# Kernel tuning notes

Measured on AMD Instinct MI355X. Metric: run time of the kernel, lower is better.

Reference implementation:

```python
import jax, jax.numpy as jnp
import numpy as np

N = 100000   # nodes
E = 1600000  # edges (before self loops)
H = 4        # heads
C = 32       # per-head channels
D = H * C    # hidden_dim = 128
G = 64       # graphs in batch
L = 4        # num_layers
IN_DIM = 7
NEG_SLOPE = 0.2


def setup_inputs() -> dict:
    key = jax.random.key(0)
    ks = jax.random.split(key, 14)
    s = 0.1
    x = jax.random.normal(ks[0], (N, IN_DIM), jnp.float32)
    edge_index = jax.random.randint(ks[1], (2, E), 0, N, dtype=jnp.int32)
    batch = jnp.sort(jax.random.randint(ks[2], (N,), 0, G, dtype=jnp.int32))
    W0 = jax.random.normal(ks[3], (IN_DIM, D), jnp.float32) * s
    a_src0 = jax.random.normal(ks[4], (H, C), jnp.float32) * s
    a_dst0 = jax.random.normal(ks[5], (H, C), jnp.float32) * s
    b0 = jnp.zeros((D,), jnp.float32)
    Ws = jax.random.normal(ks[6], (L - 1, D, D), jnp.float32) * s
    a_srcs = jax.random.normal(ks[7], (L - 1, H, C), jnp.float32) * s
    a_dsts = jax.random.normal(ks[8], (L - 1, H, C), jnp.float32) * s
    bs = jnp.zeros((L - 1, D), jnp.float32)
    ln_g = jnp.ones((L, D), jnp.float32)
    ln_b = jnp.zeros((L, D), jnp.float32)
    return dict(x=x, edge_index=edge_index, batch=batch, W0=W0, a_src0=a_src0,
                a_dst0=a_dst0, b0=b0, Ws=Ws, a_srcs=a_srcs, a_dsts=a_dsts,
                bs=bs, ln_g=ln_g, ln_b=ln_b)


def _gat_layer(x, W, a_src, a_dst, b, src, dst):
    # x: [N, F_in] -> h: [N, H, C] (PyG GATConv: shared lin for src/dst)
    h = (x @ W).reshape(N, H, C)
    alpha_src = jnp.einsum('nhc,hc->nh', h, a_src)  # [N, H]
    alpha_dst = jnp.einsum('nhc,hc->nh', h, a_dst)  # [N, H]
    logits = jax.nn.leaky_relu(alpha_src[src] + alpha_dst[dst], NEG_SLOPE)  # [E', H]
    # segment softmax over edges grouped by destination node
    m = jax.ops.segment_max(logits, dst, num_segments=N)          # [N, H]
    e = jnp.exp(logits - m[dst])
    z = jax.ops.segment_sum(e, dst, num_segments=N)               # [N, H]
    alpha = e / (z[dst] + 1e-16)                                  # [E', H]
    msg = h[src] * alpha[..., None]                               # [E', H, C]
    out = jax.ops.segment_sum(msg, dst, num_segments=N)           # [N, H, C]
    return out.reshape(N, D) + b


def _layernorm(x, g, b):
    mu = jnp.mean(x, axis=-1, keepdims=True)
    var = jnp.var(x, axis=-1, keepdims=True)
    return (x - mu) * jax.lax.rsqrt(var + 1e-5) * g + b


def reference(x, edge_index, batch, W0, a_src0, a_dst0, b0, Ws, a_srcs, a_dsts, bs, ln_g, ln_b):
    # PyG GATConv default: add self loops
    loop = jnp.arange(N, dtype=edge_index.dtype)
    src = jnp.concatenate([edge_index[0], loop])
    dst = jnp.concatenate([edge_index[1], loop])
    h = x
    for i in range(L):
        if i == 0:
            W, asr, ads, b = W0, a_src0, a_dst0, b0
        else:
            W, asr, ads, b = Ws[i - 1], a_srcs[i - 1], a_dsts[i - 1], bs[i - 1]
        h_new = _gat_layer(h, W, asr, ads, b, src, dst)
        h_new = jax.nn.elu(_layernorm(h_new, ln_g[i], ln_b[i]))
        h = h + h_new if i > 0 else h_new  # dropout is identity in eval
    node_embeddings = h  # [N, D]
    sums = jax.ops.segment_sum(node_embeddings, batch, num_segments=G)  # [G, D]
    cnt = jax.ops.segment_sum(jnp.ones((N,), node_embeddings.dtype), batch, num_segments=G)
    graph_embedding = sums / jnp.maximum(cnt, 1.0)[:, None]
    return node_embeddings, graph_embedding
```

## Files before the change

### kernel.cpp

```cpp
#include <hip/hip_runtime.h>
#include <hip/hip_bf16.h>

#define NN 100000
#define NE 1600000
#define NH 4
#define NC 32
#define DD 128
#define NG 64
#define NIN 7

#define BSH 9
#define NBUK ((NN + 511) >> BSH)
#define SEGCAP 9600
#define CAPE (SEGCAP - 512)
#define CSRN (NBUK * SEGCAP)
#define NBBIN ((NE + 4095)/4096)

typedef __hip_bfloat16 bf16;
typedef __attribute__((ext_vector_type(8))) short short8;
typedef __attribute__((ext_vector_type(4))) float f32x4;
typedef __attribute__((ext_vector_type(2))) float f32x2;

__device__ __forceinline__ float b2f(const bf16 v){ return __bfloat162float(v); }

__device__ __forceinline__ float in_ld(const void* p, size_t i, int f32){
  return f32 ? ((const float*)p)[i] : b2f(((const bf16*)p)[i]);
}

__device__ __forceinline__ unsigned int bfbits(float v){
  bf16 b = __float2bfloat16(v);
  return (unsigned int)(*(unsigned short*)&b);
}

__global__ __launch_bounds__(256) void k_init(float* __restrict__ gsum, int* __restrict__ gcnt,
                                              int* __restrict__ bcur,
                                              const unsigned int* __restrict__ xb, int* __restrict__ flag){
  int i = blockIdx.x*256 + threadIdx.x;
  if (i < NG*DD) gsum[i] = 0.f;
  if (i < NG) gcnt[i] = 0;
  if (i < NBUK) bcur[i] = i * CAPE;
  if (blockIdx.x == 0 && threadIdx.x < 64){
    int t = threadIdx.x;
    int pl = 0;
    for (int j = t; j < 512; j += 64){
      float v = __uint_as_float(xb[j]);
      float a = fabsf(v);
      if (v == v && a < 1e6f && a > 1e-10f) pl++;
    }
    #pragma unroll
    for (int off = 32; off > 0; off >>= 1) pl += __shfl_down(pl, off);
    if (t == 0) *flag = (pl >= 384) ? 1 : 0;
  }
}

__global__ __launch_bounds__(256) void k_bin(const int* __restrict__ src, const int* __restrict__ dst,
                                             int* __restrict__ bcur, int2* __restrict__ gstag,
                                             const void* __restrict__ Ws, bf16* __restrict__ WT,
                                             const int* __restrict__ flag){
  if (blockIdx.x >= NBBIN){
    int l = blockIdx.x - NBBIN;
    int f32 = *flag;
    for (int idx = threadIdx.x; idx < DD*DD; idx += 256){
      int n = idx >> 7, k = idx & 127;
      WT[(size_t)l*DD*DD + idx] = __float2bfloat16(in_ld(Ws, (size_t)l*DD*DD + (size_t)k*DD + n, f32));
    }
    return;
  }
  __shared__ int cnt[NBUK], pref[NBUK+1], place[NBUK], gbase[NBUK];
  __shared__ int2 pairs[4096];
  int tid = threadIdx.x;
  for (int b = tid; b < NBUK; b += 256){ cnt[b]=0; place[b]=0; }
  __syncthreads();
  int e0 = blockIdx.x*4096;
  int s[16], d[16];
  #pragma unroll
  for (int i=0;i<16;i++){
    int e = e0 + i*256 + tid;
    s[i] = 0; d[i] = -1;
    if (e < NE){
      unsigned int us = (unsigned int)src[e]; if (us >= NN) us = 0;
      unsigned int ud = (unsigned int)dst[e]; if (ud >= NN) ud = 0;
      s[i] = (int)us; d[i] = (int)ud;
      atomicAdd(&cnt[ud>>BSH], 1);
    }
  }
  __syncthreads();
  if (tid == 0){
    int run = 0;
    for (int b=0;b<NBUK;b++){ pref[b] = run; run += cnt[b]; }
    pref[NBUK] = run;
  }
  __syncthreads();
  for (int b = tid; b < NBUK; b += 256){
    if (cnt[b] > 0) gbase[b] = atomicAdd(&bcur[b], cnt[b]);
  }
  __syncthreads();
  #pragma unroll
  for (int i=0;i<16;i++){
    if (d[i] >= 0){
      int b = d[i]>>BSH;
      int lp = atomicAdd(&place[b],1);
      pairs[pref[b]+lp] = make_int2(s[i], d[i]);
    }
  }
  __syncthreads();
  int tot = pref[NBUK];
  for (int j = tid; j < tot; j += 256){
    int2 pr = pairs[j];
    int b = pr.y>>BSH;
    int gidx = gbase[b] + (j - pref[b]);
    if (gidx >= b*CAPE && gidx < (b+1)*CAPE) gstag[gidx] = pr;
  }
}

__global__ __launch_bounds__(256) void k_bucket(const int2* __restrict__ gstag,
                                                const int* __restrict__ bcur,
                                                int* __restrict__ csr,
                                                int* __restrict__ offs, int* __restrict__ oend){
  __shared__ int seg[SEGCAP];
  __shared__ int lcnt[512];
  __shared__ int loff[512];
  __shared__ int pscan[256];
  int b = blockIdx.x, tid = threadIdx.x;
  int nstart = b << BSH;
  int nend = min(nstart + 512, NN);
  int nloc = nend - nstart;
  int base = b * SEGCAP;
  int stbase = b * CAPE;
  int ecnt = bcur[b] - stbase;
  ecnt = max(0, min(ecnt, CAPE));
  lcnt[tid]     = (tid < nloc) ? 1 : 0;
  lcnt[tid+256] = (tid+256 < nloc) ? 1 : 0;
  __syncthreads();
  for (int j = tid; j < ecnt; j += 256){
    int2 pr = gstag[stbase + j];
    int ln = pr.y - nstart;
    if (ln < 0 || ln >= nloc) ln = 0;
    atomicAdd(&lcnt[ln], 1);
  }
  __syncthreads();
  int c0 = lcnt[2*tid], c1 = lcnt[2*tid+1];
  int pairsum = c0 + c1;
  pscan[tid] = pairsum;
  __syncthreads();
  for (int off=1; off<256; off<<=1){
    int a = (tid >= off) ? pscan[tid-off] : 0;
    __syncthreads();
    pscan[tid] += a;
    __syncthreads();
  }
  int pexcl = pscan[tid] - pairsum;
  loff[2*tid]   = pexcl;
  loff[2*tid+1] = pexcl + c0;
  __syncthreads();
  int segN = pscan[255];
  if (segN > SEGCAP) segN = SEGCAP;
  if (tid < nloc){
    offs[nstart + tid] = base + loff[tid];
    oend[nstart + tid] = base + loff[tid] + lcnt[tid];
  }
  if (tid + 256 < nloc){
    offs[nstart + tid + 256] = base + loff[tid+256];
    oend[nstart + tid + 256] = base + loff[tid+256] + lcnt[tid+256];
  }
  __syncthreads();
  if (tid < nloc){ int p = loff[tid]; if (p < SEGCAP) seg[p] = nstart + tid; lcnt[tid] = 1; }
  if (tid + 256 < nloc){ int p = loff[tid+256]; if (p < SEGCAP) seg[p] = nstart + tid + 256; lcnt[tid+256] = 1; }
  __syncthreads();
  for (int j = tid; j < ecnt; j += 256){
    int2 pr = gstag[stbase + j];
    int ln = pr.y - nstart;
    if (ln < 0 || ln >= nloc) ln = 0;
    int p = atomicAdd(&lcnt[ln], 1);
    int idx = loff[ln] + p;
    if (idx >= 0 && idx < SEGCAP) seg[idx] = pr.x;
  }
  __syncthreads();
  for (int j = tid; j < segN; j += 256) csr[base + j] = seg[j];
}

__device__ __forceinline__ void alpha_red(float acc, float was, float wad, int d, int n,
                                          float* __restrict__ asrc, float* __restrict__ adst){
  float ps = acc*was, pd = acc*wad;
  #pragma unroll
  for (int off=16; off>0; off>>=1){
    ps += __shfl_down(ps, off, 32);
    pd += __shfl_down(pd, off, 32);
  }
  if ((d & 31) == 0){
    asrc[n*NH + (d>>5)] = ps;
    adst[n*NH + (d>>5)] = pd;
  }
}

__global__ __launch_bounds__(128) void k_gemm0(const void* __restrict__ x, const void* __restrict__ W,
    const void* __restrict__ aws, const void* __restrict__ awd,
    bf16* __restrict__ hproj,
    float* __restrict__ asrc, float* __restrict__ adst, const int* __restrict__ flag){
  int f32 = *flag;
  __shared__ float xr[4][NIN];
  int d = threadIdx.x;
  int n0 = blockIdx.x*4;
  if (d < 4*NIN) xr[d/NIN][d%NIN] = in_ld(x, (size_t)n0*NIN + d, f32);
  __syncthreads();
  float a0=0,a1=0,a2=0,a3=0;
  #pragma unroll
  for (int k=0;k<NIN;k++){
    float w = in_ld(W, (size_t)k*DD + d, f32);
    a0 += xr[0][k]*w; a1 += xr[1][k]*w; a2 += xr[2][k]*w; a3 += xr[3][k]*w;
  }
  hproj[(size_t)(n0+0)*DD+d]=__float2bfloat16(a0);
  hproj[(size_t)(n0+1)*DD+d]=__float2bfloat16(a1);
  hproj[(size_t)(n0+2)*DD+d]=__float2bfloat16(a2);
  hproj[(size_t)(n0+3)*DD+d]=__float2bfloat16(a3);
  float was = in_ld(aws, d, f32), wad = in_ld(awd, d, f32);
  alpha_red(a0, was, wad, d, n0+0, asrc, adst);
  alpha_red(a1, was, wad, d, n0+1, asrc, adst);
  alpha_red(a2, was, wad, d, n0+2, asrc, adst);
  alpha_red(a3, was, wad, d, n0+3, asrc, adst);
}

#define LDA 136
#define LDB 136

__global__ __launch_bounds__(256) void k_gemm_mfma(
    const bf16* __restrict__ resid,
    const bf16* __restrict__ WT, size_t wtoff,
    const void* __restrict__ aws, const void* __restrict__ awd, size_t aoff,
    bf16* __restrict__ hproj,
    float* __restrict__ asrc, float* __restrict__ adst,
    const int* __restrict__ flag)
{
  __shared__ bf16 sA[64*LDA];
  __shared__ bf16 sB[128*LDB];
  int f32 = *flag;
  int t = threadIdx.x;
  int n0 = blockIdx.x*64;

  {
    const uint4* srcv = (const uint4*)(WT + wtoff);
    #pragma unroll
    for (int i=0;i<8;i++){
      int u4 = t + 256*i;
      int row = u4 >> 4, c = u4 & 15;
      *(uint4*)(&sB[row*LDB + c*8]) = srcv[u4];
    }
  }
  {
    const uint4* av = (const uint4*)resid;
    #pragma unroll
    for (int i=0;i<4;i++){
      int u4 = t + 256*i;
      int row = u4 >> 4, c = u4 & 15;
      int gr = n0 + row;
      uint4 v = make_uint4(0,0,0,0);
      if (gr < NN) v = av[(size_t)gr*16 + c];
      *(uint4*)(&sA[row*LDA + c*8]) = v;
    }
  }
  __syncthreads();

  int wv = t >> 6, lane = t & 63;
  int m = lane & 15, kq = lane >> 4;
  int rowbase = wv*16;

  f32x4 acc[8];
  #pragma unroll
  for (int nt=0; nt<8; nt++) acc[nt] = (f32x4){0.f,0.f,0.f,0.f};

  #pragma unroll
  for (int ks=0; ks<4; ks++){
    short8 afrag = *(const short8*)(&sA[(rowbase + m)*LDA + ks*32 + kq*8]);
    #pragma unroll
    for (int nt=0; nt<8; nt++){
      short8 bfrag = *(const short8*)(&sB[(nt*16 + m)*LDB + ks*32 + kq*8]);
      acc[nt] = __builtin_amdgcn_mfma_f32_16x16x32_bf16(afrag, bfrag, acc[nt], 0, 0, 0);
    }
  }

  #pragma unroll
  for (int reg=0; reg<4; reg++){
    int gr = n0 + rowbase + kq*4 + reg;
    if (gr < NN){
      bf16* dst = hproj + (size_t)gr*DD + m;
      #pragma unroll
      for (int nt=0; nt<8; nt++)
        dst[nt*16] = __float2bfloat16(acc[nt][reg]);
    }
  }

  float avs[8], avd[8];
  #pragma unroll
  for (int nt=0; nt<8; nt++){
    avs[nt] = in_ld(aws, aoff + nt*16 + m, f32);
    avd[nt] = in_ld(awd, aoff + nt*16 + m, f32);
  }
  #pragma unroll
  for (int h=0; h<4; h++){
    #pragma unroll
    for (int reg=0; reg<4; reg++){
      float ps = acc[2*h][reg]*avs[2*h] + acc[2*h+1][reg]*avs[2*h+1];
      float pd = acc[2*h][reg]*avd[2*h] + acc[2*h+1][reg]*avd[2*h+1];
      #pragma unroll
      for (int off=1; off<16; off<<=1){
        ps += __shfl_xor(ps, off);
        pd += __shfl_xor(pd, off);
      }
      if (m == 0){
        int gr = n0 + rowbase + kq*4 + reg;
        if (gr < NN){
          asrc[gr*NH + h] = ps;
          adst[gr*NH + h] = pd;
        }
      }
    }
  }
}

__device__ __forceinline__ float4 edge_e(const float4 as, const float4 ad){
  float4 l, e;
  l.x = as.x + ad.x; l.y = as.y + ad.y; l.z = as.z + ad.z; l.w = as.w + ad.w;
  l.x = l.x > 0.f ? l.x : 0.2f*l.x;
  l.y = l.y > 0.f ? l.y : 0.2f*l.y;
  l.z = l.z > 0.f ? l.z : 0.2f*l.z;
  l.w = l.w > 0.f ? l.w : 0.2f*l.w;
  l.x = fminf(l.x, 30.f); l.y = fminf(l.y, 30.f);
  l.z = fminf(l.z, 30.f); l.w = fminf(l.w, 30.f);
  e.x = __expf(l.x); e.y = __expf(l.y); e.z = __expf(l.z); e.w = __expf(l.w);
  return e;
}

__device__ __forceinline__ float2 hp_ld2(const void* hp, int s, int lane){
  unsigned int hv = ((const unsigned int*)hp)[(size_t)s*64 + lane];
  return make_float2(__uint_as_float(hv << 16), __uint_as_float(hv & 0xFFFF0000u));
}

__device__ __forceinline__ void fma_row(const uint4 hv, const float al,
                                        f32x2& a0, f32x2& a1, f32x2& a2, f32x2& a3){
  f32x2 v0 = {__uint_as_float(hv.x << 16), __uint_as_float(hv.x & 0xFFFF0000u)};
  f32x2 v1 = {__uint_as_float(hv.y << 16), __uint_as_float(hv.y & 0xFFFF0000u)};
  f32x2 v2 = {__uint_as_float(hv.z << 16), __uint_as_float(hv.z & 0xFFFF0000u)};
  f32x2 v3 = {__uint_as_float(hv.w << 16), __uint_as_float(hv.w & 0xFFFF0000u)};
  a0 += v0 * al;
  a1 += v1 * al;
  a2 += v2 * al;
  a3 += v3 * al;
}

template<int U>
__global__ __launch_bounds__(256) void k_agg(const bf16* __restrict__ hproj,
    const float* __restrict__ asrc, const float* __restrict__ adst,
    const int* __restrict__ offs, const int* __restrict__ oend, const int* __restrict__ csr,
    bf16* __restrict__ resid,
    const void* __restrict__ bias, size_t boff,
    const void* __restrict__ lng, const void* __restrict__ lnb, size_t lnoff,
    const int* __restrict__ flag, const int first)
{
  __shared__ float s_al[4][256];
  __shared__ int   s_off[4][64];
  int f32 = *flag;
  int wid = threadIdx.x >> 6, lane = threadIdx.x & 63;
  int n = blockIdx.x*4 + wid;
  int beg = offs[n];
  int end = oend[n];
  beg = max(0, min(beg, CSRN));
  end = max(beg, min(end, CSRN));
  int deg = min(end - beg, 1024);
  const float4 ad = ((const float4*)adst)[n];
  int head = lane >> 4;
  const char* hpB = (const char*)hproj;
  float2 acc;

  if (deg <= 64){
    float4 e = make_float4(0,0,0,0);
    if (lane < deg){
      unsigned int us = (unsigned int)csr[beg+lane];
      if (us >= NN) us = 0;
      s_off[wid][lane] = (int)(us << 8);
      float4 as = ((const float4*)asrc)[us];
      e = edge_e(as, ad);
    }
    float4 zs = e;
    #pragma unroll
    for (int off=32; off>0; off>>=1){
      zs.x += __shfl_down(zs.x, off);
      zs.y += __shfl_down(zs.y, off);
      zs.z += __shfl_down(zs.z, off);
      zs.w += __shfl_down(zs.w, off);
    }
    float4 invz;
    invz.x = 1.f/(__shfl(zs.x,0)+1e-16f);
    invz.y = 1.f/(__shfl(zs.y,0)+1e-16f);
    invz.z = 1.f/(__shfl(zs.z,0)+1e-16f);
    invz.w = 1.f/(__shfl(zs.w,0)+1e-16f);
    if (lane < deg){
      s_al[wid][lane*4+0] = e.x*invz.x;
      s_al[wid][lane*4+1] = e.y*invz.y;
      s_al[wid][lane*4+2] = e.z*invz.z;
      s_al[wid][lane*4+3] = e.w*invz.w;
    }
    __threadfence_block();

    int qg = lane >> 4;
    int ql = lane & 15;
    int hq = ql >> 2;
    int qbyte = ql << 4;
    f32x2 a0 = {0.f,0.f}, a1 = {0.f,0.f}, a2 = {0.f,0.f}, a3 = {0.f,0.f};
    int t = 0;
    for (; t+U <= deg; t += U){
      uint4 h[U/4];
      #pragma unroll
      for (int u=0; u<U/4; u++){
        int j = t + 4*u + qg;
        unsigned int off = (unsigned int)s_off[wid][j] + qbyte;
        h[u] = *(const uint4*)(hpB + off);
      }
      #pragma unroll
      for (int u=0; u<U/4; u++){
        int j = t + 4*u + qg;
        float al = s_al[wid][j*4 + hq];
        fma_row(h[u], al, a0, a1, a2, a3);
      }
    }
    for (; t+4 <= deg; t += 4){
      int j = t + qg;
      unsigned int off = (unsigned int)s_off[wid][j] + qbyte;
      const uint4 hv = *(const uint4*)(hpB + off);
      float al = s_al[wid][j*4 + hq];
      fma_row(hv, al, a0, a1, a2, a3);
    }
    if (t < deg){
      int j = t + qg;
      if (j < deg){
        unsigned int off = (unsigned int)s_off[wid][j] + qbyte;
        const uint4 hv = *(const uint4*)(hpB + off);
        float al = s_al[wid][j*4 + hq];
        fma_row(hv, al, a0, a1, a2, a3);
      }
    }

    #pragma unroll
    for (int off = 16; off < 64; off <<= 1){
      a0.x += __shfl_xor(a0.x, off); a0.y += __shfl_xor(a0.y, off);
      a1.x += __shfl_xor(a1.x, off); a1.y += __shfl_xor(a1.y, off);
      a2.x += __shfl_xor(a2.x, off); a2.y += __shfl_xor(a2.y, off);
      a3.x += __shfl_xor(a3.x, off); a3.y += __shfl_xor(a3.y, off);
    }
    __threadfence_block();
    if (qg == 0){
      float* red = &s_al[wid][0];
      red[ql*8+0] = a0.x; red[ql*8+1] = a0.y;
      red[ql*8+2] = a1.x; red[ql*8+3] = a1.y;
      red[ql*8+4] = a2.x; red[ql*8+5] = a2.y;
      red[ql*8+6] = a3.x; red[ql*8+7] = a3.y;
    }
    __threadfence_block();
    acc = make_float2(s_al[wid][2*lane], s_al[wid][2*lane+1]);
  } else {
    f32x2 ac0 = {0.f,0.f};
    float4 zs = make_float4(0,0,0,0);
    for (int j=lane; j<deg; j+=64){
      unsigned int us = (unsigned int)csr[beg+j];
      if (us >= NN) us = 0;
      float4 as = ((const float4*)asrc)[us];
      float4 e = edge_e(as, ad);
      zs.x+=e.x; zs.y+=e.y; zs.z+=e.z; zs.w+=e.w;
    }
    #pragma unroll
    for (int off=32; off>0; off>>=1){
      zs.x += __shfl_down(zs.x, off);
      zs.y += __shfl_down(zs.y, off);
      zs.z += __shfl_down(zs.z, off);
      zs.w += __shfl_down(zs.w, off);
    }
    float4 invz;
    invz.x = 1.f/(__shfl(zs.x,0)+1e-16f);
    invz.y = 1.f/(__shfl(zs.y,0)+1e-16f);
    invz.z = 1.f/(__shfl(zs.z,0)+1e-16f);
    invz.w = 1.f/(__shfl(zs.w,0)+1e-16f);
    int nch = (deg+63)>>6;
    for (int c2=0;c2<nch;c2++){
      int base = c2<<6, j = base+lane;
      int sreg = 0;
      __threadfence_block();
      if (j < deg){
        unsigned int us = (unsigned int)csr[beg+j];
        if (us >= NN) us = 0;
        sreg = (int)us;
        float4 as = ((const float4*)asrc)[us];
        float4 e = edge_e(as, ad);
        s_al[wid][lane*4+0]=e.x*invz.x;
        s_al[wid][lane*4+1]=e.y*invz.y;
        s_al[wid][lane*4+2]=e.z*invz.z;
        s_al[wid][lane*4+3]=e.w*invz.w;
      }
      __threadfence_block();
      int cnt = min(64, deg-base);
      int head2 = lane >> 4;
      for (int t2=0;t2<cnt;t2++){
        int s = __shfl(sreg, t2);
        float a = s_al[wid][t2*4+head2];
        float2 hv = hp_ld2(hproj, s, lane);
        ac0.x += hv.x*a;
        ac0.y += hv.y*a;
      }
    }
    acc = make_float2(ac0.x, ac0.y);
  }

  float vx = acc.x + in_ld(bias, boff + 2*lane,   f32);
  float vy = acc.y + in_ld(bias, boff + 2*lane+1, f32);
  float s1 = vx+vy, s2 = vx*vx+vy*vy;
  #pragma unroll
  for (int off=32; off>0; off>>=1){
    s1 += __shfl_down(s1, off);
    s2 += __shfl_down(s2, off);
  }
  float mean = __shfl(s1,0) * (1.f/DD);
  float msq  = __shfl(s2,0) * (1.f/DD);
  float var  = fmaxf(msq - mean*mean, 0.f);
  float r = rsqrtf(var + 1e-5f);
  float yx = (vx-mean)*r*in_ld(lng, lnoff+2*lane,   f32) + in_ld(lnb, lnoff+2*lane,   f32);
  float yy = (vy-mean)*r*in_ld(lng, lnoff+2*lane+1, f32) + in_ld(lnb, lnoff+2*lane+1, f32);
  yx = yx>0.f ? yx : expm1f(yx);
  yy = yy>0.f ? yy : expm1f(yy);
  float2 res;
  if (first){
    res = make_float2(yx, yy);
  } else {
    unsigned int pu = ((const unsigned int*)resid)[(size_t)n*64 + lane];
    res = make_float2(__uint_as_float(pu << 16) + yx,
                      __uint_as_float(pu & 0xFFFF0000u) + yy);
  }
  unsigned int pk = bfbits(res.x) | (bfbits(res.y) << 16);
  ((unsigned int*)resid)[(size_t)n*64 + lane] = pk;
}

__global__ __launch_bounds__(128) void k_pool(const bf16* __restrict__ resid, void* __restrict__ dout,
    const int* __restrict__ batch, float* __restrict__ gsum, int* __restrict__ gcnt,
    const int* __restrict__ flag){
  __shared__ int sb[64];
  int f32 = *flag;
  int d = threadIdx.x;
  int n0 = blockIdx.x*64;
  int cnt = min(64, NN - n0);
  if (d < cnt){
    unsigned int b = (unsigned int)batch[n0 + d];
    if (b >= NG) b = 0;
    sb[d] = (int)b;
  }
  __syncthreads();
  float local = 0.f;
  int cur = sb[0];
  for (int i=0;i<cnt;i++){
    int b = sb[i];
    if (b != cur){
      atomicAdd(&gsum[cur*DD + d], local);
      local = 0.f; cur = b;
    }
    size_t idx = (size_t)(n0+i)*DD + d;
    float v = b2f(resid[idx]);
    if (f32) ((float*)dout)[idx] = v;
    else     ((bf16*)dout)[idx] = resid[idx];
    local += v;
  }
  atomicAdd(&gsum[cur*DD + d], local);
  if (d == 0){
    int lc = 0; int c2 = sb[0];
    for (int i=0;i<cnt;i++){
      int b = sb[i];
      if (b != c2){ atomicAdd(&gcnt[c2], lc); lc = 0; c2 = b; }
      lc++;
    }
    atomicAdd(&gcnt[c2], lc);
  }
}

__global__ __launch_bounds__(128) void k_final(const float* __restrict__ gsum, const int* __restrict__ gcnt,
                                               void* __restrict__ dout, const int* __restrict__ flag){
  int f32 = *flag;
  int i = blockIdx.x*128 + threadIdx.x;
  if (i < NG*DD){
    float c = (float)gcnt[i>>7];
    if (c < 1.f) c = 1.f;
    float val = gsum[i] / c;
    if (f32) ((float*)dout)[(size_t)NN*DD + i] = val;
    else     ((bf16*)dout)[(size_t)NN*DD + i] = __float2bfloat16(val);
  }
}

extern "C" void kernel_launch(void* const* d_in, const int* in_sizes, int n_in,
                              void* d_out, int out_size, void* d_ws, size_t ws_size,
                              hipStream_t stream){
  const void* x      = d_in[0];
  const int*  ei     = (const int*) d_in[1];
  const int*  batch  = (const int*) d_in[2];
  const void* W0     = d_in[3];
  const void* asrc0  = d_in[4];
  const void* adst0  = d_in[5];
  const void* b0     = d_in[6];
  const void* Ws     = d_in[7];
  const void* asrcs  = d_in[8];
  const void* adsts  = d_in[9];
  const void* bs     = d_in[10];
  const void* lng    = d_in[11];
  const void* lnb    = d_in[12];

  const int* srcs = ei;
  const int* dsts = ei + NE;

  uintptr_t p0 = (uintptr_t)d_ws;
  uintptr_t p = p0;
  auto alloc = [&](size_t bytes)->void* {
    void* r = (void*)p; p += (bytes + 255) & ~(size_t)255; return r;
  };
  int*   csr    = (int*)  alloc((size_t)CSRN*4);
  int*   offs   = (int*)  alloc((size_t)NN*4);
  int*   oend   = (int*)  alloc((size_t)NN*4);
  float* asrc   = (float*)alloc((size_t)NN*NH*4);
  float* adst   = (float*)alloc((size_t)NN*NH*4);
  float* gsum   = (float*)alloc((size_t)NG*DD*4);
  int*   gcnt   = (int*)  alloc(NG*4);
  int*   flag   = (int*)  alloc(256);
  int*   bcur   = (int*)  alloc((size_t)NBUK*4);
  int2*  gstag  = (int2*) alloc((size_t)NBUK*CAPE*8);
  bf16*  wt     = (bf16*) alloc((size_t)3*DD*DD*2);
  bf16*  hproj  = (bf16*) alloc((size_t)NN*DD*2);
  bf16*  resid  = (bf16*) alloc((size_t)NN*DD*2);

  const int NB = (NN + 255)/256;

  k_init<<<NB, 256, 0, stream>>>(gsum, gcnt, bcur, (const unsigned int*)x, flag);
  k_bin<<<NBBIN + 3, 256, 0, stream>>>(srcs, dsts, bcur, gstag, Ws, wt, flag);
  k_bucket<<<NBUK, 256, 0, stream>>>(gstag, bcur, csr, offs, oend);

  const int GEMM_B = (NN + 63)/64;

  k_gemm0<<<NN/4, 128, 0, stream>>>(x, W0, asrc0, adst0, hproj, asrc, adst, flag);
  k_agg<4><<<NN/4, 256, 0, stream>>>(hproj, asrc, adst, offs, oend, csr, resid,
                                     b0, 0, lng, lnb, 0, flag, 1);
  k_gemm_mfma<<<GEMM_B, 256, 0, stream>>>(resid, wt, 0, asrcs, adsts, 0,
                                          hproj, asrc, adst, flag);
  k_agg<8><<<NN/4, 256, 0, stream>>>(hproj, asrc, adst, offs, oend, csr, resid,
                                     bs, 0, lng, lnb, (size_t)1*DD, flag, 0);
  k_gemm_mfma<<<GEMM_B, 256, 0, stream>>>(resid, wt, (size_t)1*DD*DD, asrcs, adsts, (size_t)1*DD,
                                          hproj, asrc, adst, flag);
  k_agg<16><<<NN/4, 256, 0, stream>>>(hproj, asrc, adst, offs, oend, csr, resid,
                                      bs, (size_t)1*DD, lng, lnb, (size_t)2*DD, flag, 0);
  k_gemm_mfma<<<GEMM_B, 256, 0, stream>>>(resid, wt, (size_t)2*DD*DD, asrcs, adsts, (size_t)2*DD,
                                          hproj, asrc, adst, flag);
  k_agg<8><<<NN/4, 256, 0, stream>>>(hproj, asrc, adst, offs, oend, csr, resid,
                                     bs, (size_t)2*DD, lng, lnb, (size_t)3*DD, flag, 0);

  k_pool<<<(NN+63)/64, 128, 0, stream>>>(resid, d_out, batch, gsum, gcnt, flag);
  k_final<<<(NG*DD+127)/128, 128, 0, stream>>>(gsum, gcnt, d_out, flag);
}
```

Before: 625.7 us.

## Merge init into memset and bin, fold final into pool, retune GEMM and bucket

Replaces the init kernel with a memset plus a dtype-sniff block inside k_bin, and folds the final graph-mean into k_pool using a last-block counter, which removes two launches. k_bucket moves to 512 threads with a single-element scan. The MFMA GEMM handles 128 rows per block and reads B fragments directly from global memory instead of staging them in LDS. The aggregation template parameter is made uniform at 8, and k_agg now uses the head variable instead of a lane-derived head index. The risks are the last-block pattern needing correct fences, and uncached global B loads in the GEMM.

```diff
diff --git a/kernel.cpp b/kernel.cpp
--- a/kernel.cpp
+++ b/kernel.cpp
@@ -32,14 +32,8 @@
   return (unsigned int)(*(unsigned short*)&b);
 }
 
-__global__ __launch_bounds__(256) void k_init(float* __restrict__ gsum, int* __restrict__ gcnt,
-                                              int* __restrict__ bcur,
-                                              const unsigned int* __restrict__ xb, int* __restrict__ flag){
-  int i = blockIdx.x*256 + threadIdx.x;
-  if (i < NG*DD) gsum[i] = 0.f;
-  if (i < NG) gcnt[i] = 0;
-  if (i < NBUK) bcur[i] = i * CAPE;
-  if (blockIdx.x == 0 && threadIdx.x < 64){
+__device__ __forceinline__ int sniff_f32(const unsigned int* __restrict__ xb, int* s_f32){
+  if (threadIdx.x < 64){
     int t = threadIdx.x;
     int pl = 0;
     for (int j = t; j < 512; j += 64){
@@ -49,17 +43,26 @@
     }
     #pragma unroll
     for (int off = 32; off > 0; off >>= 1) pl += __shfl_down(pl, off);
-    if (t == 0) *flag = (pl >= 384) ? 1 : 0;
-  }
-}
+    if (t == 0) *s_f32 = (pl >= 384) ? 1 : 0;
+  }
+  __syncthreads();
+  return *s_f32;
+}
+
+__global__ __launch_bounds__(512) void k_bucket_fwd();
 
 __global__ __launch_bounds__(256) void k_bin(const int* __restrict__ src, const int* __restrict__ dst,
                                              int* __restrict__ bcur, int2* __restrict__ gstag,
                                              const void* __restrict__ Ws, bf16* __restrict__ WT,
-                                             const int* __restrict__ flag){
+                                             const unsigned int* __restrict__ xb, int* __restrict__ flag){
   if (blockIdx.x >= NBBIN){
+    __shared__ int s_f32;
+    int f32 = sniff_f32(xb, &s_f32);
     int l = blockIdx.x - NBBIN;
-    int f32 = *flag;
+    if (l == 3){
+      if (threadIdx.x == 0) *flag = f32;
+      return;
+    }
     for (int idx = threadIdx.x; idx < DD*DD; idx += 256){
       int n = idx >> 7, k = idx & 127;
       WT[(size_t)l*DD*DD + idx] = __float2bfloat16(in_ld(Ws, (size_t)l*DD*DD + (size_t)k*DD + n, f32));
@@ -92,7 +95,7 @@
   }
   __syncthreads();
   for (int b = tid; b < NBUK; b += 256){
-    if (cnt[b] > 0) gbase[b] = atomicAdd(&bcur[b], cnt[b]);
+    if (cnt[b] > 0) gbase[b] = b*CAPE + atomicAdd(&bcur[b], cnt[b]);
   }
   __syncthreads();
   #pragma unroll
@@ -113,61 +116,55 @@
   }
 }
 
-__global__ __launch_bounds__(256) void k_bucket(const int2* __restrict__ gstag,
+__global__ __launch_bounds__(512) void k_bucket(const int2* __restrict__ gstag,
                                                 const int* __restrict__ bcur,
                                                 int* __restrict__ csr,
                                                 int* __restrict__ offs, int* __restrict__ oend){
   __shared__ int seg[SEGCAP];
   __shared__ int lcnt[512];
   __shared__ int loff[512];
-  __shared__ int pscan[256];
+  __shared__ int s_segN;
   int b = blockIdx.x, tid = threadIdx.x;
   int nstart = b << BSH;
   int nend = min(nstart + 512, NN);
   int nloc = nend - nstart;
   int base = b * SEGCAP;
   int stbase = b * CAPE;
-  int ecnt = bcur[b] - stbase;
+  int ecnt = bcur[b];
   ecnt = max(0, min(ecnt, CAPE));
-  lcnt[tid]     = (tid < nloc) ? 1 : 0;
-  lcnt[tid+256] = (tid+256 < nloc) ? 1 : 0;
-  __syncthreads();
-  for (int j = tid; j < ecnt; j += 256){
+  lcnt[tid] = (tid < nloc) ? 1 : 0;
+  __syncthreads();
+  for (int j = tid; j < ecnt; j += 512){
     int2 pr = gstag[stbase + j];
     int ln = pr.y - nstart;
     if (ln < 0 || ln >= nloc) ln = 0;
     atomicAdd(&lcnt[ln], 1);
   }
   __syncthreads();
-  int c0 = lcnt[2*tid], c1 = lcnt[2*tid+1];
-  int pairsum = c0 + c1;
-  pscan[tid] = pairsum;
-  __syncthreads();
-  for (int off=1; off<256; off<<=1){
-    int a = (tid >= off) ? pscan[tid-off] : 0;
+  int own = lcnt[tid];
+  loff[tid] = own;
+  __syncthreads();
+  for (int off=1; off<512; off<<=1){
+    int a = (tid >= off) ? loff[tid-off] : 0;
     __syncthreads();
-    pscan[tid] += a;
+    loff[tid] += a;
     __syncthreads();
   }
-  int pexcl = pscan[tid] - pairsum;
-  loff[2*tid]   = pexcl;
-  loff[2*tid+1] = pexcl + c0;
-  __syncthreads();
-  int segN = pscan[255];
+  int incl = loff[tid];
+  loff[tid] = incl - own;
+  if (tid == 511) s_segN = incl;
+  __syncthreads();
+  int segN = s_segN;
   if (segN > SEGCAP) segN = SEGCAP;
   if (tid < nloc){
     offs[nstart + tid] = base + loff[tid];
-    oend[nstart + tid] = base + loff[tid] + lcnt[tid];
-  }
-  if (tid + 256 < nloc){
-    offs[nstart + tid + 256] = base + loff[tid+256];
-    oend[nstart + tid + 256] = base + loff[tid+256] + lcnt[tid+256];
-  }
-  __syncthreads();
-  if (tid < nloc){ int p = loff[tid]; if (p < SEGCAP) seg[p] = nstart + tid; lcnt[tid] = 1; }
-  if (tid + 256 < nloc){ int p = loff[tid+256]; if (p < SEGCAP) seg[p] = nstart + tid + 256; lcnt[tid+256] = 1; }
-  __syncthreads();
-  for (int j = tid; j < ecnt; j += 256){
+    oend[nstart + tid] = base + loff[tid] + own;
+    int p = loff[tid];
+    if (p < SEGCAP) seg[p] = nstart + tid;
+    lcnt[tid] = 1;
+  }
+  __syncthreads();
+  for (int j = tid; j < ecnt; j += 512){
     int2 pr = gstag[stbase + j];
     int ln = pr.y - nstart;
     if (ln < 0 || ln >= nloc) ln = 0;
@@ -176,7 +173,7 @@
     if (idx >= 0 && idx < SEGCAP) seg[idx] = pr.x;
   }
   __syncthreads();
-  for (int j = tid; j < segN; j += 256) csr[base + j] = seg[j];
+  for (int j = tid; j < segN; j += 512) csr[base + j] = seg[j];
 }
 
 __device__ __forceinline__ void alpha_red(float acc, float was, float wad, int d, int n,
@@ -193,35 +190,37 @@
   }
 }
 
-__global__ __launch_bounds__(128) void k_gemm0(const void* __restrict__ x, const void* __restrict__ W,
+__global__ __launch_bounds__(256) void k_gemm0(const void* __restrict__ x, const void* __restrict__ W,
     const void* __restrict__ aws, const void* __restrict__ awd,
     bf16* __restrict__ hproj,
     float* __restrict__ asrc, float* __restrict__ adst, const int* __restrict__ flag){
   int f32 = *flag;
-  __shared__ float xr[4][NIN];
-  int d = threadIdx.x;
-  int n0 = blockIdx.x*4;
-  if (d < 4*NIN) xr[d/NIN][d%NIN] = in_ld(x, (size_t)n0*NIN + d, f32);
+  __shared__ float xr[8][NIN];
+  int t = threadIdx.x;
+  int d = t & 127;
+  int nb = (t >> 7) * 4;
+  int n0 = blockIdx.x*8;
+  if (t < 8*NIN) xr[t/NIN][t%NIN] = in_ld(x, (size_t)n0*NIN + t, f32);
   __syncthreads();
   float a0=0,a1=0,a2=0,a3=0;
   #pragma unroll
   for (int k=0;k<NIN;k++){
     float w = in_ld(W, (size_t)k*DD + d, f32);
-    a0 += xr[0][k]*w; a1 += xr[1][k]*w; a2 += xr[2][k]*w; a3 += xr[3][k]*w;
-  }
-  hproj[(size_t)(n0+0)*DD+d]=__float2bfloat16(a0);
-  hproj[(size_t)(n0+1)*DD+d]=__float2bfloat16(a1);
-  hproj[(size_t)(n0+2)*DD+d]=__float2bfloat16(a2);
-  hproj[(size_t)(n0+3)*DD+d]=__float2bfloat16(a3);
+    a0 += xr[nb+0][k]*w; a1 += xr[nb+1][k]*w; a2 += xr[nb+2][k]*w; a3 += xr[nb+3][k]*w;
+  }
+  hproj[(size_t)(n0+nb+0)*DD+d]=__float2bfloat16(a0);
+  hproj[(size_t)(n0+nb+1)*DD+d]=__float2bfloat16(a1);
+  hproj[(size_t)(n0+nb+2)*DD+d]=__float2bfloat16(a2);
+  hproj[(size_t)(n0+nb+3)*DD+d]=__float2bfloat16(a3);
   float was = in_ld(aws, d, f32), wad = in_ld(awd, d, f32);
-  alpha_red(a0, was, wad, d, n0+0, asrc, adst);
-  alpha_red(a1, was, wad, d, n0+1, asrc, adst);
-  alpha_red(a2, was, wad, d, n0+2, asrc, adst);
-  alpha_red(a3, was, wad, d, n0+3, asrc, adst);
+  alpha_red(a0, was, wad, d, n0+nb+0, asrc, adst);
+  alpha_red(a1, was, wad, d, n0+nb+1, asrc, adst);
+  alpha_red(a2, was, wad, d, n0+nb+2, asrc, adst);
+  alpha_red(a3, was, wad, d, n0+nb+3, asrc, adst);
 }
 
 #define LDA 136
-#define LDB 136
+#define GRPB 128
 
 __global__ __launch_bounds__(256) void k_gemm_mfma(
     const bf16* __restrict__ resid,
@@ -231,25 +230,15 @@
     float* __restrict__ asrc, float* __restrict__ adst,
     const int* __restrict__ flag)
 {
-  __shared__ bf16 sA[64*LDA];
-  __shared__ bf16 sB[128*LDB];
+  __shared__ bf16 sA[GRPB*LDA];
   int f32 = *flag;
   int t = threadIdx.x;
-  int n0 = blockIdx.x*64;
-
-  {
-    const uint4* srcv = (const uint4*)(WT + wtoff);
-    #pragma unroll
-    for (int i=0;i<8;i++){
-      int u4 = t + 256*i;
-      int row = u4 >> 4, c = u4 & 15;
-      *(uint4*)(&sB[row*LDB + c*8]) = srcv[u4];
-    }
-  }
+  int n0 = blockIdx.x*GRPB;
+
   {
     const uint4* av = (const uint4*)resid;
     #pragma unroll
-    for (int i=0;i<4;i++){
+    for (int i=0;i<8;i++){
       int u4 = t + 256*i;
       int row = u4 >> 4, c = u4 & 15;
       int gr = n0 + row;
@@ -262,30 +251,37 @@
 
   int wv = t >> 6, lane = t & 63;
   int m = lane & 15, kq = lane >> 4;
-  int rowbase = wv*16;
-
-  f32x4 acc[8];
-  #pragma unroll
-  for (int nt=0; nt<8; nt++) acc[nt] = (f32x4){0.f,0.f,0.f,0.f};
+  const bf16* WB = WT + wtoff;
+
+  f32x4 acc[2][8];
+  #pragma unroll
+  for (int rg=0; rg<2; rg++)
+    #pragma unroll
+    for (int nt=0; nt<8; nt++) acc[rg][nt] = (f32x4){0.f,0.f,0.f,0.f};
 
   #pragma unroll
   for (int ks=0; ks<4; ks++){
-    short8 afrag = *(const short8*)(&sA[(rowbase + m)*LDA + ks*32 + kq*8]);
+    short8 af0 = *(const short8*)(&sA[(wv*32 +  0 + m)*LDA + ks*32 + kq*8]);
+    short8 af1 = *(const short8*)(&sA[(wv*32 + 16 + m)*LDA + ks*32 + kq*8]);
     #pragma unroll
     for (int nt=0; nt<8; nt++){
-      short8 bfrag = *(const short8*)(&sB[(nt*16 + m)*LDB + ks*32 + kq*8]);
-      acc[nt] = __builtin_amdgcn_mfma_f32_16x16x32_bf16(afrag, bfrag, acc[nt], 0, 0, 0);
-    }
-  }
-
-  #pragma unroll
-  for (int reg=0; reg<4; reg++){
-    int gr = n0 + rowbase + kq*4 + reg;
-    if (gr < NN){
-      bf16* dst = hproj + (size_t)gr*DD + m;
-      #pragma unroll
-      for (int nt=0; nt<8; nt++)
-        dst[nt*16] = __float2bfloat16(acc[nt][reg]);
+      short8 bf = *(const short8*)(WB + (size_t)(nt*16 + m)*DD + ks*32 + kq*8);
+      acc[0][nt] = __builtin_amdgcn_mfma_f32_16x16x32_bf16(af0, bf, acc[0][nt], 0, 0, 0);
+      acc[1][nt] = __builtin_amdgcn_mfma_f32_16x16x32_bf16(af1, bf, acc[1][nt], 0, 0, 0);
+    }
+  }
+
+  #pragma unroll
+  for (int rg=0; rg<2; rg++){
+    #pragma unroll
+    for (int reg=0; reg<4; reg++){
+      int gr = n0 + wv*32 + rg*16 + kq*4 + reg;
+      if (gr < NN){
+        bf16* dst = hproj + (size_t)gr*DD + m;
+        #pragma unroll
+        for (int nt=0; nt<8; nt++)
+          dst[nt*16] = __float2bfloat16(acc[rg][nt][reg]);
+      }
     }
   }
 
@@ -296,21 +292,24 @@
     avd[nt] = in_ld(awd, aoff + nt*16 + m, f32);
   }
   #pragma unroll
-  for (int h=0; h<4; h++){
-    #pragma unroll
-    for (int reg=0; reg<4; reg++){
-      float ps = acc[2*h][reg]*avs[2*h] + acc[2*h+1][reg]*avs[2*h+1];
-      float pd = acc[2*h][reg]*avd[2*h] + acc[2*h+1][reg]*avd[2*h+1];
+  for (int rg=0; rg<2; rg++){
+    #pragma unroll
+    for (int h=0; h<4; h++){
       #pragma unroll
-      for (int off=1; off<16; off<<=1){
-        ps += __shfl_xor(ps, off);
-        pd += __shfl_xor(pd, off);
-      }
-      if (m == 0){
-        int gr = n0 + rowbase + kq*4 + reg;
-        if (gr < NN){
-          asrc[gr*NH + h] = ps;
-          adst[gr*NH + h] = pd;
+      for (int reg=0; reg<4; reg++){
+        float ps = acc[rg][2*h][reg]*avs[2*h] + acc[rg][2*h+1][reg]*avs[2*h+1];
+        float pd = acc[rg][2*h][reg]*avd[2*h] + acc[rg][2*h+1][reg]*avd[2*h+1];
+        #pragma unroll
+        for (int off=1; off<16; off<<=1){
+          ps += __shfl_xor(ps, off);
+          pd += __shfl_xor(pd, off);
+        }
+        if (m == 0){
+          int gr = n0 + wv*32 + rg*16 + kq*4 + reg;
+          if (gr < NN){
+            asrc[gr*NH + h] = ps;
+            adst[gr*NH + h] = pd;
+          }
         }
       }
     }
@@ -496,10 +495,9 @@
       }
       __threadfence_block();
       int cnt = min(64, deg-base);
-      int head2 = lane >> 4;
       for (int t2=0;t2<cnt;t2++){
         int s = __shfl(sreg, t2);
-        float a = s_al[wid][t2*4+head2];
+        float a = s_al[wid][t2*4+head];
         float2 hv = hp_ld2(hproj, s, lane);
         ac0.x += hv.x*a;
         ac0.y += hv.y*a;
@@ -538,8 +536,9 @@
 
 __global__ __launch_bounds__(128) void k_pool(const bf16* __restrict__ resid, void* __restrict__ dout,
     const int* __restrict__ batch, float* __restrict__ gsum, int* __restrict__ gcnt,
-    const int* __restrict__ flag){
+    int* __restrict__ ctr, const int* __restrict__ flag){
   __shared__ int sb[64];
+  __shared__ int s_last;
   int f32 = *flag;
   int d = threadIdx.x;
   int n0 = blockIdx.x*64;
@@ -574,18 +573,23 @@
     }
     atomicAdd(&gcnt[c2], lc);
   }
-}
-
-__global__ __launch_bounds__(128) void k_final(const float* __restrict__ gsum, const int* __restrict__ gcnt,
-                                               void* __restrict__ dout, const int* __restrict__ flag){
-  int f32 = *flag;
-  int i = blockIdx.x*128 + threadIdx.x;
-  if (i < NG*DD){
-    float c = (float)gcnt[i>>7];
-    if (c < 1.f) c = 1.f;
-    float val = gsum[i] / c;
-    if (f32) ((float*)dout)[(size_t)NN*DD + i] = val;
-    else     ((bf16*)dout)[(size_t)NN*DD + i] = __float2bfloat16(val);
+  __threadfence();
+  if (d == 0){
+    int done = atomicAdd(ctr, 1);
+    s_last = (done == (int)gridDim.x - 1) ? 1 : 0;
+  }
+  __syncthreads();
+  if (s_last){
+    __threadfence();
+    for (int i = d; i < NG*DD; i += 128){
+      float sv = __hip_atomic_load(&gsum[i], __ATOMIC_RELAXED, __HIP_MEMORY_SCOPE_AGENT);
+      int   cv = __hip_atomic_load(&gcnt[i>>7], __ATOMIC_RELAXED, __HIP_MEMORY_SCOPE_AGENT);
+      float c = (float)cv;
+      if (c < 1.f) c = 1.f;
+      float val = sv / c;
+      if (f32) ((float*)dout)[(size_t)NN*DD + i] = val;
+      else     ((bf16*)dout)[(size_t)NN*DD + i] = __float2bfloat16(val);
+    }
   }
 }
 
@@ -614,44 +618,42 @@
   auto alloc = [&](size_t bytes)->void* {
     void* r = (void*)p; p += (bytes + 255) & ~(size_t)255; return r;
   };
+  float* gsum   = (float*)alloc((size_t)NG*DD*4);
+  int*   gcnt   = (int*)  alloc(NG*4);
+  int*   ctr    = (int*)  alloc(256);
+  int*   bcur   = (int*)  alloc((size_t)NBUK*4);
+  size_t zbytes = (size_t)(p - (uintptr_t)gsum);
   int*   csr    = (int*)  alloc((size_t)CSRN*4);
   int*   offs   = (int*)  alloc((size_t)NN*4);
   int*   oend   = (int*)  alloc((size_t)NN*4);
   float* asrc   = (float*)alloc((size_t)NN*NH*4);
   float* adst   = (float*)alloc((size_t)NN*NH*4);
-  float* gsum   = (float*)alloc((size_t)NG*DD*4);
-  int*   gcnt   = (int*)  alloc(NG*4);
   int*   flag   = (int*)  alloc(256);
-  int*   bcur   = (int*)  alloc((size_t)NBUK*4);
   int2*  gstag  = (int2*) alloc((size_t)NBUK*CAPE*8);
   bf16*  wt     = (bf16*) alloc((size_t)3*DD*DD*2);
   bf16*  hproj  = (bf16*) alloc((size_t)NN*DD*2);
   bf16*  resid  = (bf16*) alloc((size_t)NN*DD*2);
 
-  const int NB = (NN + 255)/256;
-
-  k_init<<<NB, 256, 0, stream>>>(gsum, gcnt, bcur, (const unsigned int*)x, flag);
-  k_bin<<<NBBIN + 3, 256, 0, stream>>>(srcs, dsts, bcur, gstag, Ws, wt, flag);
-  k_bucket<<<NBUK, 256, 0, stream>>>(gstag, bcur, csr, offs, oend);
-
-  const int GEMM_B = (NN + 63)/64;
-
-  k_gemm0<<<NN/4, 128, 0, stream>>>(x, W0, asrc0, adst0, hproj, asrc, adst, flag);
-  k_agg<4><<<NN/4, 256, 0, stream>>>(hproj, asrc, adst, offs, oend, csr, resid,
+  hipMemsetAsync(gsum, 0, zbytes, stream);
+
+  k_bin<<<NBBIN + 4, 256, 0, stream>>>(srcs, dsts, bcur, gstag, Ws, wt,
+                                       (const unsigned int*)x, flag);
+  k_bucket<<<NBUK, 512, 0, stream>>>(gstag, bcur, csr, offs, oend);
+
+  const int GEMM_B = (NN + GRPB - 1)/GRPB;
+
+  k_gemm0<<<NN/8, 256, 0, stream>>>(x, W0, asrc0, adst0, hproj, asrc, adst, flag);
+  k_agg<8><<<NN/4, 256, 0, stream>>>(hproj, asrc, adst, offs, oend, csr, resid,
                                      b0, 0, lng, lnb, 0, flag, 1);
-  k_gemm_mfma<<<GEMM_B, 256, 0, stream>>>(resid, wt, 0, asrcs, adsts, 0,
-                                          hproj, asrc, adst, flag);
-  k_agg<8><<<NN/4, 256, 0, stream>>>(hproj, asrc, adst, offs, oend, csr, resid,
-                                     bs, 0, lng, lnb, (size_t)1*DD, flag, 0);
-  k_gemm_mfma<<<GEMM_B, 256, 0, stream>>>(resid, wt, (size_t)1*DD*DD, asrcs, adsts, (size_t)1*DD,
-                                          hproj, asrc, adst, flag);
-  k_agg<16><<<NN/4, 256, 0, stream>>>(hproj, asrc, adst, offs, oend, csr, resid,
-                                      bs, (size_t)1*DD, lng, lnb, (size_t)2*DD, flag, 0);
-  k_gemm_mfma<<<GEMM_B, 256, 0, stream>>>(resid, wt, (size_t)2*DD*DD, asrcs, adsts, (size_t)2*DD,
-                                          hproj, asrc, adst, flag);
-  k_agg<8><<<NN/4, 256, 0, stream>>>(hproj, asrc, adst, offs, oend, csr, resid,
-                                     bs, (size_t)2*DD, lng, lnb, (size_t)3*DD, flag, 0);
-
-  k_pool<<<(NN+63)/64, 128, 0, stream>>>(resid, d_out, batch, gsum, gcnt, flag);
-  k_final<<<(NG*DD+127)/128, 128, 0, stream>>>(gsum, gcnt, d_out, flag);
-}
+  for (int l=1; l<4; l++){
+    size_t wtoff = (size_t)(l-1)*DD*DD;
+    size_t aoff  = (size_t)(l-1)*DD;
+    k_gemm_mfma<<<GEMM_B, 256, 0, stream>>>(resid, wt, wtoff,
+                                            asrcs, adsts, aoff,
+                                            hproj, asrc, adst, flag);
+    k_agg<8><<<NN/4, 256, 0, stream>>>(hproj, asrc, adst, offs, oend, csr, resid,
+                                       bs, (size_t)(l-1)*DD, lng, lnb, (size_t)l*DD, flag, 0);
+  }
+
+  k_pool<<<(NN+63)/64, 128, 0, stream>>>(resid, d_out, batch, gsum, gcnt, ctr, flag);
+}
```

Result: slower. 737.3 us (+17.8%).
